# Performance work log

Measured on AMD Instinct MI355X. Metric: run time of the kernel, lower is better.

## Reference

```python
import jax, jax.numpy as jnp
import numpy as np

B, H, W, C = 16, 224, 224, 3
NP = 14                      # n_patches per side
PH = PW = H // NP            # 16
PATCH = PH * PW * C          # 768
D_MODEL = 512
EXPAND = 2
D_INNER = D_MODEL * EXPAND   # 1024
D_STATE = 16
D_CONV = 4
DT_RANK = -(-D_MODEL // 16)  # ceil(512/16) = 32
N_LAYERS = 4
N_CLASSES = 1000


def posemb_sincos_2d(h, w, dim, temperature=10000.0):
    y, x = jnp.meshgrid(jnp.arange(h, dtype=jnp.float32), jnp.arange(w, dtype=jnp.float32), indexing='ij')
    omega = jnp.arange(dim // 4, dtype=jnp.float32) / (dim // 4 - 1)
    omega = 1.0 / (temperature ** omega)
    yy = y.reshape(-1, 1) * omega[None, :]
    xx = x.reshape(-1, 1) * omega[None, :]
    return jnp.concatenate([jnp.sin(xx), jnp.cos(xx), jnp.sin(yy), jnp.cos(yy)], axis=1)  # [h*w, dim]


def setup_inputs() -> dict:
    key = jax.random.key(0)
    ks = jax.random.split(key, 12)
    s = 0.02
    inp = {
        'x': jax.random.normal(ks[0], (B, H, W, C), jnp.float32),
        'patch_w': jax.random.normal(ks[1], (PATCH, D_MODEL), jnp.float32) * s,
        'patch_b': jnp.zeros((D_MODEL,), jnp.float32),
        'norm_w': jnp.ones((N_LAYERS, D_MODEL), jnp.float32),
        'in_proj_w': jax.random.normal(ks[2], (N_LAYERS, D_MODEL, 2 * D_INNER), jnp.float32) * s,
        'conv_w': jax.random.normal(ks[3], (N_LAYERS, D_INNER, D_CONV), jnp.float32) * 0.1,
        'x_proj_w': jax.random.normal(ks[4], (N_LAYERS, D_INNER, DT_RANK + 2 * D_STATE), jnp.float32) * s,
        'dt_proj_w': jax.random.normal(ks[5], (N_LAYERS, DT_RANK, D_INNER), jnp.float32) * s,
        'dt_proj_b': jax.random.normal(ks[6], (N_LAYERS, D_INNER), jnp.float32) * 0.1,
        'A_log': jnp.broadcast_to(jnp.log(jnp.arange(1, D_STATE + 1, dtype=jnp.float32)), (N_LAYERS, D_INNER, D_STATE)) + 0.0,
        'D': jnp.ones((N_LAYERS, D_INNER), jnp.float32),
        'out_proj_w': jax.random.normal(ks[7], (N_LAYERS, D_INNER, D_MODEL), jnp.float32) * s,
        'head_w': jax.random.normal(ks[8], (D_MODEL, N_CLASSES), jnp.float32) * s,
        'head_b': jnp.zeros((N_CLASSES,), jnp.float32),
    }
    return inp


def rms_norm(x, w, eps=1e-5):
    return x * jax.lax.rsqrt(jnp.mean(x * x, axis=-1, keepdims=True) + eps) * w


def selective_scan(u, delta, A, Bm, Cm, Dv):
    # u, delta: [b,l,d]; A: [d,n]; Bm, Cm: [b,l,n]; Dv: [d]
    dA = jnp.exp(jnp.einsum('bld,dn->bldn', delta, A))          # [b,l,d,n]
    dBu = jnp.einsum('bld,bln->bldn', delta * u, Bm)            # [b,l,d,n]
    b, l, d = u.shape
    n = A.shape[1]

    def step(s, inp):
        dA_t, dBu_t, C_t = inp
        s = dA_t * s + dBu_t                                    # [b,d,n]
        y = jnp.einsum('bdn,bn->bd', s, C_t)
        return s, y

    s0 = jnp.zeros((b, d, n), u.dtype)
    _, ys = jax.lax.scan(step, s0, (dA.transpose(1, 0, 2, 3), dBu.transpose(1, 0, 2, 3), Cm.transpose(1, 0, 2)))
    y = ys.transpose(1, 0, 2)                                   # [b,l,d]
    return y + u * Dv


def mamba_block(x, in_w, conv_w, xp_w, dt_w, dt_b, A_log, Dv, out_w):
    b, l, _ = x.shape
    xr = x @ in_w                                               # [b,l,2*d_inner]
    xi, res = jnp.split(xr, 2, axis=-1)
    # causal depthwise conv over sequence
    xc = jax.lax.conv_general_dilated(
        xi.transpose(0, 2, 1),                                  # [b,d_inner,l]
        conv_w[:, None, :],                                     # [d_inner,1,k]
        window_strides=(1,), padding=[(D_CONV - 1, 0)],
        feature_group_count=D_INNER,
        dimension_numbers=('NCH', 'OIH', 'NCH'))
    xi = jax.nn.silu(xc.transpose(0, 2, 1))                     # [b,l,d_inner]
    A = -jnp.exp(A_log)
    x_dbl = xi @ xp_w                                           # [b,l,dt_rank+2n]
    delta, Bm, Cm = jnp.split(x_dbl, [DT_RANK, DT_RANK + D_STATE], axis=-1)
    delta = jax.nn.softplus(delta @ dt_w + dt_b)                # [b,l,d_inner]
    y = selective_scan(xi, delta, A, Bm, Cm, Dv)
    y = y * jax.nn.silu(res)
    return y @ out_w


def reference(x, patch_w, patch_b, norm_w, in_proj_w, conv_w, x_proj_w, dt_proj_w, dt_proj_b, A_log, D, out_proj_w, head_w, head_b):
    b = x.shape[0]
    # patchify: b (h ph) (w pw) c -> b (h w) (ph pw c)
    p = x.reshape(b, NP, PH, NP, PW, C).transpose(0, 1, 3, 2, 4, 5).reshape(b, NP * NP, PATCH)
    h = p @ patch_w + patch_b                                   # [b, 196, d_model]
    h = h + posemb_sincos_2d(NP, NP, D_MODEL)[None]
    for i in range(N_LAYERS):
        h = h + mamba_block(rms_norm(h, norm_w[i]), in_proj_w[i], conv_w[i], x_proj_w[i],
                            dt_proj_w[i], dt_proj_b[i], A_log[i], D[i], out_proj_w[i])
    h = h.mean(axis=1)                                          # [b, d_model]
    return h @ head_w + head_b                                  # [b, n_classes]
```

## Files before the change

### kernel.cpp

```cpp
#include <hip/hip_runtime.h>
#include <hip/hip_bf16.h>
#include <math.h>

#define BATCH 16
#define L_SEQ 196
#define PATCH_DIM 768
#define D_MODEL 512
#define D_INNER 1024
#define D_STATE 16
#define D_CONV 4
#define DT_RANK 32
#define N_LAYERS 4
#define N_CLASSES 1000
#define ROWS (BATCH * L_SEQ)
#define ROWSP 3200
#define NBIG 1152

typedef __hip_bfloat16 bf16;
typedef __attribute__((ext_vector_type(8))) __bf16 bf16x8;
typedef __attribute__((ext_vector_type(8))) short short8;
typedef __attribute__((ext_vector_type(4))) float f32x4;

__device__ __forceinline__ void gload_lds16(const void* g, void* l) {
    __builtin_amdgcn_global_load_lds((const __attribute__((address_space(1))) void*)g,
                                     (__attribute__((address_space(3))) void*)l, 16, 0, 0);
}
__device__ __forceinline__ float bfbits2f(int b) {
    return __int_as_float(((unsigned)b & 0xFFFFu) << 16);
}
__device__ __forceinline__ unsigned short f2bfbits(float f) {
    __hip_bfloat16 h = __float2bfloat16(f);
    return *reinterpret_cast<unsigned short*>(&h);
}

__global__ void posemb_kernel(float* __restrict__ pos) {
    int idx = blockIdx.x * 256 + threadIdx.x;
    if (idx >= L_SEQ * D_MODEL) return;
    int l = idx >> 9, col = idx & 511;
    int q = col >> 7, wi = col & 127;
    float omega = powf(10000.f, -(float)wi / 127.f);
    float yv = (float)(l / 14), xv = (float)(l % 14);
    float arg = (q < 2 ? xv : yv) * omega;
    pos[idx] = (q & 1) ? cosf(arg) : sinf(arg);
}

__global__ void patchify_kernel(const float* __restrict__ x, bf16* __restrict__ p) {
    int idx = blockIdx.x * 256 + threadIdx.x;
    if (idx >= ROWS * PATCH_DIM) return;
    int k = idx % PATCH_DIM, row = idx / PATCH_DIM;
    int b = row / L_SEQ, l = row % L_SEQ;
    int i = l / 14, j = l % 14;
    int ph = k / 48, r = k % 48, pw = r / 3, c = r % 3;
    size_t src = (((size_t)b * 224 + i * 16 + ph) * 224 + (j * 16 + pw)) * 3 + c;
    p[idx] = __float2bfloat16(x[src]);
}

__global__ __launch_bounds__(256) void transpose_bf16_kernel(
    const float* __restrict__ src, bf16* __restrict__ dst,
    int K, int N, int Npad, size_t src_lstride, size_t dst_lstride)
{
    src += (size_t)blockIdx.z * src_lstride;
    dst += (size_t)blockIdx.z * dst_lstride;
    __shared__ float tile[32][33];
    int kb = blockIdx.y * 32, nb = blockIdx.x * 32;
    int tx = threadIdx.x & 31, ty = threadIdx.x >> 5;
    #pragma unroll
    for (int i = 0; i < 4; ++i) {
        int k = kb + ty + 8 * i, n = nb + tx;
        tile[ty + 8 * i][tx] = (k < K && n < N) ? src[(size_t)k * N + n] : 0.f;
    }
    __syncthreads();
    #pragma unroll
    for (int i = 0; i < 4; ++i) {
        int n = nb + ty + 8 * i, k = kb + tx;
        if (n < Npad && k < K) dst[(size_t)n * K + k] = __float2bfloat16(tile[tx][ty + 8 * i]);
    }
}

__global__ __launch_bounds__(256) void wcomb_kernel(
    const float* __restrict__ xpw_all,
    const float* __restrict__ dtw_all,
    bf16* __restrict__ WtBig_all)
{
    int z = blockIdx.z;
    const float* xpw = xpw_all + (size_t)z * D_INNER * 64;
    const float* dtw = dtw_all + (size_t)z * DT_RANK * D_INNER;
    bf16* Wt = WtBig_all + (size_t)z * NBIG * D_INNER;
    __shared__ float sd[32][17];
    __shared__ float sx[16][33];
    int n0 = blockIdx.x * 16, k0 = blockIdx.y * 16;
    int tid = threadIdx.x;
    {
        int e = tid;        sd[e >> 4][e & 15] = dtw[(e >> 4) * D_INNER + n0 + (e & 15)];
        e = tid + 256;      sd[e >> 4][e & 15] = dtw[(e >> 4) * D_INNER + n0 + (e & 15)];
    }
    {
        int e = tid;        sx[e >> 5][e & 31] = xpw[(size_t)(k0 + (e >> 5)) * 64 + (e & 31)];
        e = tid + 256;      sx[e >> 5][e & 31] = xpw[(size_t)(k0 + (e >> 5)) * 64 + (e & 31)];
    }
    __syncthreads();
    int nn = tid >> 4, kk = tid & 15;
    float acc = 0.f;
    #pragma unroll
    for (int r = 0; r < 32; ++r) acc += sd[r][nn] * sx[kk][r];
    Wt[(size_t)(n0 + nn) * D_INNER + k0 + kk] = __float2bfloat16(acc);
}

__global__ void bcw_kernel(const float* __restrict__ xpw_all, bf16* __restrict__ WtBig_all) {
    int z = blockIdx.y;
    const float* xpw = xpw_all + (size_t)z * D_INNER * 64;
    bf16* WtBig = WtBig_all + (size_t)z * NBIG * D_INNER;
    int idx = blockIdx.x * 256 + threadIdx.x;
    if (idx >= 32 * 1024) return;
    int j = idx >> 10, k = idx & 1023;
    int src = (j & 1) ? 48 + (j >> 1) : 32 + (j >> 1);
    WtBig[(size_t)(1024 + j) * 1024 + k] = __float2bfloat16(xpw[k * 64 + src]);
}

__global__ void cwt_kernel(const float* __restrict__ cw, float* __restrict__ cwT) {
    int z = blockIdx.y;
    int idx = blockIdx.x * 256 + threadIdx.x;
    if (idx >= 4096) return;
    int d = idx >> 2, k = idx & 3;
    cwT[(size_t)z * 4096 + k * 1024 + d] = cw[(size_t)z * 4096 + d * 4 + k];
}

template<int MODE, int BM>
__global__ __launch_bounds__(256) void gemm64(
    const bf16* __restrict__ A, const bf16* __restrict__ Wt,
    int K, int gx, int Nstore, int M, int ldc,
    float* __restrict__ Cf, bf16* __restrict__ Cb,
    const float* __restrict__ bias, const float* __restrict__ pos,
    float* __restrict__ Cf2)
{
    constexpr int MI = BM / 32;
    constexpr int NL = 4 + 2 * MI;
    int nwg = gridDim.x, bid = blockIdx.x;
    int q = nwg >> 3, r = nwg & 7;
    int xcd = bid & 7, sub = bid >> 3;
    int wgid = (xcd < r ? xcd * (q + 1) : r * (q + 1) + (xcd - r) * q) + sub;
    int bx = wgid % gx, by = wgid / gx;
    int bm = by * BM, bn = bx * 128;

    __shared__ short Als[2][BM * 64];
    __shared__ short Bls[2][128 * 64];
    int tid = threadIdx.x;
    int lane = tid & 63, wid = tid >> 6;
    int wm = wid >> 1, wn = wid & 1;

    int t3 = tid >> 3, t7 = tid & 7;
    int rA0 = t3,      kA0 = t7 ^ (rA0 & 7);
    int rA1 = 32 + t3, kA1 = t7 ^ (rA1 & 7);
    const bf16* gA0 = A + (size_t)(bm + rA0) * K + kA0 * 8;
    const bf16* gA1 = A + (size_t)(bm + rA1) * K + kA1 * 8;
    const int aB0 = (wid * 64) * 8, aB1 = (256 + wid * 64) * 8;
    int rB0 = t3,      kB0 = t7 ^ (rB0 & 7);
    int rB1 = 32 + t3, kB1 = t7 ^ (rB1 & 7);
    int rB2 = 64 + t3, kB2 = t7 ^ (rB2 & 7);
    int rB3 = 96 + t3, kB3 = t7 ^ (rB3 & 7);
    const bf16* gB0 = Wt + (size_t)(bn + rB0) * K + kB0 * 8;
    const bf16* gB1 = Wt + (size_t)(bn + rB1) * K + kB1 * 8;
    const bf16* gB2 = Wt + (size_t)(bn + rB2) * K + kB2 * 8;
    const bf16* gB3 = Wt + (size_t)(bn + rB3) * K + kB3 * 8;
    const int bB0 = (wid * 64) * 8,       bB1 = (256 + wid * 64) * 8;
    const int bB2 = (512 + wid * 64) * 8, bB3 = (768 + wid * 64) * 8;

    auto stage = [&](int buf, int k0) {
        gload_lds16(gA0 + k0, &Als[buf][aB0]);
        if (BM == 64) gload_lds16(gA1 + k0, &Als[buf][aB1]);
        gload_lds16(gB0 + k0, &Bls[buf][bB0]);
        gload_lds16(gB1 + k0, &Bls[buf][bB1]);
        gload_lds16(gB2 + k0, &Bls[buf][bB2]);
        gload_lds16(gB3 + k0, &Bls[buf][bB3]);
    };

    f32x4 acc[MI][4];
    #pragma unroll
    for (int i = 0; i < MI; ++i)
        #pragma unroll
        for (int j = 0; j < 4; ++j)
            acc[i][j] = (f32x4){0.f, 0.f, 0.f, 0.f};

    stage(0, 0);
    int cur = 0;
    for (int k0 = 0; k0 < K; k0 += 64) {
        if (k0 + 64 < K) {
            stage(cur ^ 1, k0 + 64);
            __builtin_amdgcn_sched_barrier(0);
            asm volatile("s_waitcnt vmcnt(%0)" :: "n"(NL) : "memory");
        } else {
            asm volatile("s_waitcnt vmcnt(0)" ::: "memory");
        }
        __builtin_amdgcn_s_barrier();
        __builtin_amdgcn_sched_barrier(0);

        bf16x8 af[2][MI], bfr[2][4];
        #pragma unroll
        for (int kw = 0; kw < 2; ++kw) {
            int kc = kw * 4 + (lane >> 4);
            #pragma unroll
            for (int mi = 0; mi < MI; ++mi) {
                int row = wm * (BM / 2) + mi * 16 + (lane & 15);
                int kbp = kc ^ (row & 7);
                af[kw][mi] = *reinterpret_cast<const bf16x8*>(&Als[cur][row * 64 + kbp * 8]);
            }
            #pragma unroll
            for (int nj = 0; nj < 4; ++nj) {
                int row = wn * 64 + nj * 16 + (lane & 15);
                int kbp = kc ^ (row & 7);
                bfr[kw][nj] = *reinterpret_cast<const bf16x8*>(&Bls[cur][row * 64 + kbp * 8]);
            }
        }
        #pragma unroll
        for (int kw = 0; kw < 2; ++kw)
            #pragma unroll
            for (int mi = 0; mi < MI; ++mi)
                #pragma unroll
                for (int nj = 0; nj < 4; ++nj)
                    acc[mi][nj] = __builtin_amdgcn_mfma_f32_16x16x32_bf16(af[kw][mi], bfr[kw][nj], acc[mi][nj], 0, 0, 0);

        __builtin_amdgcn_sched_barrier(0);
        __builtin_amdgcn_s_barrier();
        cur ^= 1;
    }

    #pragma unroll
    for (int mi = 0; mi < MI; ++mi) {
        #pragma unroll
        for (int nj = 0; nj < 4; ++nj) {
            int r0 = bm + wm * (BM / 2) + mi * 16 + ((lane >> 4) << 2);
            int col = bn + wn * 64 + nj * 16 + (lane & 15);
            if (col >= Nstore) continue;
            #pragma unroll
            for (int j = 0; j < 4; ++j) {
                int row = r0 + j;
                if (row >= M) continue;
                float v = acc[mi][nj][j];
                if (MODE == 4) {
                    if (col < 1024) {
                        float z = v + bias[col];
                        Cf[(size_t)row * 1024 + col] = (z > 20.f) ? z : log1pf(__expf(z));
                    } else {
                        Cf2[(size_t)row * 32 + (col - 1024)] = v;
                    }
                } else {
                    size_t o = (size_t)row * ldc + col;
                    if (MODE == 0) Cb[o] = __float2bfloat16(v);
                    else if (MODE == 2) Cf[o] = v + bias[col] + pos[(size_t)(row % L_SEQ) * D_MODEL + col];
                    else if (MODE == 3) Cf[o] += v;
                }
            }
        }
    }
}

__global__ __launch_bounds__(256) void rmsnorm_kernel(
    const float* __restrict__ h, const float* __restrict__ w, bf16* __restrict__ o)
{
    int row = blockIdx.x;
    int tid = threadIdx.x;
    const float* hr = h + (size_t)row * D_MODEL;
    float v0 = hr[tid], v1 = hr[tid + 256];
    float ss = v0 * v0 + v1 * v1;
    #pragma unroll
    for (int off = 32; off; off >>= 1) ss += __shfl_down(ss, off);
    __shared__ float ls[4];
    __shared__ float scale_s;
    if ((tid & 63) == 0) ls[tid >> 6] = ss;
    __syncthreads();
    if (tid == 0) {
        float t = ls[0] + ls[1] + ls[2] + ls[3];
        scale_s = rsqrtf(t * (1.f / D_MODEL) + 1e-5f);
    }
    __syncthreads();
    float sc = scale_s;
    o[(size_t)row * D_MODEL + tid]       = __float2bfloat16(v0 * sc * w[tid]);
    o[(size_t)row * D_MODEL + tid + 256] = __float2bfloat16(v1 * sc * w[tid + 256]);
}

__global__ __launch_bounds__(256) void conv_silu_kernel(
    const bf16* __restrict__ xr, const float* __restrict__ cwT,
    bf16* __restrict__ xs, unsigned int* __restrict__ ug)
{
    int idx = blockIdx.x * 256 + threadIdx.x;
    if (idx >= ROWS * 128) return;
    int dg = idx & 127, row = idx >> 7;
    int d0 = dg << 3;
    int l = row % L_SEQ;
    float acc[8] = {0.f,0.f,0.f,0.f,0.f,0.f,0.f,0.f};
    #pragma unroll
    for (int k = 0; k < 4; ++k) {
        int ls = l - 3 + k;
        if (ls < 0) continue;
        short8 xv = *reinterpret_cast<const short8*>(xr + (size_t)(row - 3 + k) * 2048 + d0);
        const float* wk = cwT + k * 1024 + d0;
        #pragma unroll
        for (int j = 0; j < 8; ++j)
            acc[j] += bfbits2f(xv[j]) * wk[j];
    }
    short8 rv = *reinterpret_cast<const short8*>(xr + (size_t)row * 2048 + 1024 + d0);
    short8 xsv;
    unsigned ugv[8];
    #pragma unroll
    for (int j = 0; j < 8; ++j) {
        float u = acc[j] / (1.f + __expf(-acc[j]));
        unsigned short ub = f2bfbits(u);
        xsv[j] = (short)ub;
        float res = bfbits2f(rv[j]);
        float g = res / (1.f + __expf(-res));
        ugv[j] = (unsigned)ub | ((unsigned)f2bfbits(g) << 16);
    }
    *reinterpret_cast<short8*>(xs + (size_t)row * 1024 + d0) = xsv;
    uint4* up = reinterpret_cast<uint4*>(ug + (size_t)row * 1024 + d0);
    up[0] = make_uint4(ugv[0], ugv[1], ugv[2], ugv[3]);
    up[1] = make_uint4(ugv[4], ugv[5], ugv[6], ugv[7]);
}

__global__ __launch_bounds__(256) void scan_sp_kernel(
    const unsigned int* __restrict__ ug,
    const float* __restrict__ delta,
    const float* __restrict__ bc,
    const float* __restrict__ A_log,
    const float* __restrict__ Dv,
    bf16* __restrict__ y)
{
    int tid = threadIdx.x;
    int n2 = tid & 7, ch = tid >> 3;
    int b = blockIdx.x >> 5;
    int d = (((int)blockIdx.x & 31) << 5) | ch;
    size_t bbase = (size_t)b * L_SEQ;

    const float L2E = 1.4426950408889634f;
    float A0 = -__expf(A_log[d * 16 + 2 * n2]) * L2E;
    float A1 = -__expf(A_log[d * 16 + 2 * n2 + 1]) * L2E;
    float Dd = Dv[d];
    float s0 = 0.f, s1 = 0.f;

    const unsigned* pu = ug + bbase * 1024 + d;
    const float*    pd = delta + bbase * 1024 + d;
    const float*    pb = bc + bbase * 32 + 4 * n2;
    bf16*           py = y + bbase * 1024 + d;

    unsigned uv[8];
    float dlv[8];
    f32x4 bcv[8];

#define LOADSLOT(i) { \
    uv[i]  = pu[(i) * 1024]; \
    dlv[i] = pd[(i) * 1024]; \
    bcv[i] = *reinterpret_cast<const f32x4*>(pb + (i) * 32); }

#define STEP(i) { \
    float _dl = dlv[i]; \
    float _u  = __int_as_float(uv[i] << 16); \
    float _a0 = __builtin_amdgcn_exp2f(_dl * A0); \
    float _a1 = __builtin_amdgcn_exp2f(_dl * A1); \
    float _du = _dl * _u; \
    s0 = _a0 * s0 + _du * bcv[i].x; \
    s1 = _a1 * s1 + _du * bcv[i].z; \
    float _p = s0 * bcv[i].y + s1 * bcv[i].w; \
    _p += __int_as_float(__builtin_amdgcn_mov_dpp(__float_as_int(_p), 0xB1, 0xF, 0xF, true)); \
    _p += __int_as_float(__builtin_amdgcn_mov_dpp(__float_as_int(_p), 0x4E, 0xF, 0xF, true)); \
    _p += __int_as_float(__builtin_amdgcn_mov_dpp(__float_as_int(_p), 0x141, 0xF, 0xF, true)); \
    if (n2 == 0) { \
        float _g = __int_as_float(uv[i] & 0xFFFF0000u); \
        py[(i) * 1024] = __float2bfloat16((_p + _u * Dd) * _g); \
    } }

    LOADSLOT(0) LOADSLOT(1) LOADSLOT(2) LOADSLOT(3)
    LOADSLOT(4) LOADSLOT(5) LOADSLOT(6) LOADSLOT(7)
    pu += 8 * 1024; pd += 8 * 1024; pb += 8 * 32;

    for (int g = 0; g < 23; ++g) {
        STEP(0) LOADSLOT(0)
        STEP(1) LOADSLOT(1)
        STEP(2) LOADSLOT(2)
        STEP(3) LOADSLOT(3)
        STEP(4) LOADSLOT(4)
        STEP(5) LOADSLOT(5)
        STEP(6) LOADSLOT(6)
        STEP(7) LOADSLOT(7)
        pu += 8 * 1024; pd += 8 * 1024; pb += 8 * 32; py += 8 * 1024;
    }
    STEP(0) LOADSLOT(0)
    STEP(1) LOADSLOT(1)
    STEP(2) LOADSLOT(2)
    STEP(3) LOADSLOT(3)
    STEP(4) STEP(5) STEP(6) STEP(7)
    py += 8 * 1024;
    STEP(0) STEP(1) STEP(2) STEP(3)
#undef LOADSLOT
#undef STEP
}

__global__ __launch_bounds__(256) void mean_kernel(const float* __restrict__ h,
                                                   float* __restrict__ hm) {
    int c = blockIdx.x * 256 + threadIdx.x;
    int b = blockIdx.y;
    const float* hb = h + (size_t)b * L_SEQ * D_MODEL + c;
    float acc = 0.f;
    #pragma unroll 4
    for (int l = 0; l < L_SEQ; ++l) acc += hb[(size_t)l * D_MODEL];
    hm[b * D_MODEL + c] = acc * (1.f / L_SEQ);
}

__global__ __launch_bounds__(256) void head_kernel(
    const float* __restrict__ hm, const float* __restrict__ head_w,
    const float* __restrict__ head_b, float* __restrict__ out)
{
    __shared__ float hmr[D_MODEL];
    int tid = threadIdx.x;
    int b = blockIdx.y;
    hmr[tid]       = hm[b * D_MODEL + tid];
    hmr[tid + 256] = hm[b * D_MODEL + tid + 256];
    __syncthreads();
    int c = blockIdx.x * 256 + tid;
    if (c >= N_CLASSES) return;
    float acc = head_b[c];
    #pragma unroll 8
    for (int k = 0; k < D_MODEL; ++k)
        acc += hmr[k] * head_w[(size_t)k * N_CLASSES + c];
    out[(size_t)b * N_CLASSES + c] = acc;
}

extern "C" void kernel_launch(void* const* d_in, const int* in_sizes, int n_in,
                              void* d_out, int out_size, void* d_ws, size_t ws_size,
                              hipStream_t stream) {
    const float* x         = (const float*)d_in[0];
    const float* patch_w   = (const float*)d_in[1];
    const float* patch_b   = (const float*)d_in[2];
    const float* norm_w    = (const float*)d_in[3];
    const float* in_proj_w = (const float*)d_in[4];
    const float* conv_w    = (const float*)d_in[5];
    const float* x_proj_w  = (const float*)d_in[6];
    const float* dt_proj_w = (const float*)d_in[7];
    const float* dt_proj_b = (const float*)d_in[8];
    const float* A_log     = (const float*)d_in[9];
    const float* Dv        = (const float*)d_in[10];
    const float* out_proj_w= (const float*)d_in[11];
    const float* head_w    = (const float*)d_in[12];
    const float* head_b    = (const float*)d_in[13];
    float* out = (float*)d_out;

    char* base = (char*)d_ws;
    size_t off = 0;
    auto alloc = [&](size_t bytes) -> void* {
        void* p = base + off;
        off += (bytes + 255) & ~(size_t)255;
        return p;
    };
    float* pos   = (float*)alloc((size_t)L_SEQ * D_MODEL * 4);
    bf16*  pwT   = (bf16*) alloc((size_t)D_MODEL * PATCH_DIM * 2);
    bf16*  inT   = (bf16*) alloc((size_t)N_LAYERS * 2 * D_INNER * D_MODEL * 2);
    bf16*  WtBig = (bf16*) alloc((size_t)N_LAYERS * NBIG * D_INNER * 2);
    bf16*  opT   = (bf16*) alloc((size_t)N_LAYERS * D_MODEL * D_INNER * 2);
    float* cwT   = (float*)alloc((size_t)N_LAYERS * 4 * D_INNER * 4);
    float* h     = (float*)alloc((size_t)ROWS * D_MODEL * 4);
    bf16*  xn    = (bf16*) alloc((size_t)ROWSP * D_MODEL * 2);
    char*  reg0  = (char*) alloc((size_t)ROWSP * 2 * D_INNER * 2);
    bf16*  p     = (bf16*)reg0;
    bf16*  xr    = (bf16*)reg0;
    bf16*  xs    = (bf16*) alloc((size_t)ROWSP * D_INNER * 2);
    unsigned int* ug = (unsigned int*)alloc((size_t)ROWSP * D_INNER * 4);
    float* delta = (float*)alloc((size_t)ROWSP * D_INNER * 4);
    float* bcb   = (float*)alloc((size_t)ROWS * 32 * 4);
    bf16*  yb    = (bf16*) alloc((size_t)ROWSP * D_INNER * 2);
    float* hm    = (float*)alloc((size_t)BATCH * D_MODEL * 4);

    posemb_kernel<<<(L_SEQ * D_MODEL + 255) / 256, 256, 0, stream>>>(pos);
    patchify_kernel<<<(ROWS * PATCH_DIM + 255) / 256, 256, 0, stream>>>(x, p);
    transpose_bf16_kernel<<<dim3(16, 24), 256, 0, stream>>>(
        patch_w, pwT, PATCH_DIM, D_MODEL, D_MODEL, 0, 0);
    transpose_bf16_kernel<<<dim3(64, 16, N_LAYERS), 256, 0, stream>>>(
        in_proj_w, inT, D_MODEL, 2 * D_INNER, 2 * D_INNER,
        (size_t)D_MODEL * 2 * D_INNER, (size_t)2 * D_INNER * D_MODEL);
    transpose_bf16_kernel<<<dim3(16, 32, N_LAYERS), 256, 0, stream>>>(
        out_proj_w, opT, D_INNER, D_MODEL, D_MODEL,
        (size_t)D_INNER * D_MODEL, (size_t)D_MODEL * D_INNER);
    wcomb_kernel<<<dim3(64, 64, N_LAYERS), 256, 0, stream>>>(
        x_proj_w, dt_proj_w, WtBig);
    bcw_kernel<<<dim3(128, N_LAYERS), 256, 0, stream>>>(x_proj_w, WtBig);
    cwt_kernel<<<dim3(16, N_LAYERS), 256, 0, stream>>>(conv_w, cwT);

    gemm64<2, 32><<<(D_MODEL / 128) * (ROWSP / 32), 256, 0, stream>>>(
        p, pwT, PATCH_DIM, D_MODEL / 128, D_MODEL, ROWS, D_MODEL,
        h, nullptr, patch_b, pos, nullptr);

    for (int layer = 0; layer < N_LAYERS; ++layer) {
        rmsnorm_kernel<<<ROWS, 256, 0, stream>>>(h, norm_w + layer * D_MODEL, xn);

        gemm64<0, 64><<<(2 * D_INNER / 128) * (ROWSP / 64), 256, 0, stream>>>(
            xn, inT + (size_t)layer * 2 * D_INNER * D_MODEL,
            D_MODEL, 2 * D_INNER / 128, 2 * D_INNER, ROWS, 2 * D_INNER,
            nullptr, xr, nullptr, nullptr, nullptr);

        conv_silu_kernel<<<(ROWS * 128 + 255) / 256, 256, 0, stream>>>(
            xr, cwT + (size_t)layer * 4 * D_INNER, xs, ug);

        gemm64<4, 64><<<(NBIG / 128) * (ROWSP / 64), 256, 0, stream>>>(
            xs, WtBig + (size_t)layer * NBIG * D_INNER,
            D_INNER, NBIG / 128, 1056, ROWS, 0,
            delta, nullptr, dt_proj_b + (size_t)layer * D_INNER, nullptr, bcb);

        scan_sp_kernel<<<BATCH * (D_INNER / 32), 256, 0, stream>>>(
            ug, delta, bcb,
            A_log + (size_t)layer * D_INNER * D_STATE,
            Dv + (size_t)layer * D_INNER, yb);

        gemm64<3, 32><<<(D_MODEL / 128) * (ROWSP / 32), 256, 0, stream>>>(
            yb, opT + (size_t)layer * D_MODEL * D_INNER,
            D_INNER, D_MODEL / 128, D_MODEL, ROWS, D_MODEL,
            h, nullptr, nullptr, nullptr, nullptr);
    }

    mean_kernel<<<dim3(2, BATCH), 256, 0, stream>>>(h, hm);
    head_kernel<<<dim3(4, BATCH), 256, 0, stream>>>(hm, head_w, head_b, out);
}
```

Measured before the change: 552.6 us.

## Triple-buffer GEMM LDS staging and merge small prep kernels into one launch

The GEMM's K loop moves from double buffering to a three-stage LDS ring, with loads issued two steps ahead and vmcnt waits adjusted to match. This is meant to hide global-to-LDS latency better, at the cost of 1.5x the shared memory per block, which may reduce occupancy. Separately, the posemb, bcw and cwt setup kernels are folded into one launch to cut launch overhead. The NL count of outstanding loads is hardcoded to 6 or 5, which matches the number of loads each stage issues.

Measured after the change: 546.0 us. About the same (-1.2%).

```diff
diff --git a/kernel.cpp b/kernel.cpp
--- a/kernel.cpp
+++ b/kernel.cpp
@@ -33,17 +33,6 @@
     return *reinterpret_cast<unsigned short*>(&h);
 }
 
-__global__ void posemb_kernel(float* __restrict__ pos) {
-    int idx = blockIdx.x * 256 + threadIdx.x;
-    if (idx >= L_SEQ * D_MODEL) return;
-    int l = idx >> 9, col = idx & 511;
-    int q = col >> 7, wi = col & 127;
-    float omega = powf(10000.f, -(float)wi / 127.f);
-    float yv = (float)(l / 14), xv = (float)(l % 14);
-    float arg = (q < 2 ? xv : yv) * omega;
-    pos[idx] = (q & 1) ? cosf(arg) : sinf(arg);
-}
-
 __global__ void patchify_kernel(const float* __restrict__ x, bf16* __restrict__ p) {
     int idx = blockIdx.x * 256 + threadIdx.x;
     if (idx >= ROWS * PATCH_DIM) return;
@@ -53,6 +42,37 @@
     int ph = k / 48, r = k % 48, pw = r / 3, c = r % 3;
     size_t src = (((size_t)b * 224 + i * 16 + ph) * 224 + (j * 16 + pw)) * 3 + c;
     p[idx] = __float2bfloat16(x[src]);
+}
+
+__global__ void smallprep_kernel(float* __restrict__ pos,
+                                 const float* __restrict__ xpw_all,
+                                 bf16* __restrict__ WtBig_all,
+                                 const float* __restrict__ cw,
+                                 float* __restrict__ cwT) {
+    int bid = blockIdx.x, tid = threadIdx.x;
+    if (bid < 392) {
+        int idx = bid * 256 + tid;
+        if (idx >= L_SEQ * D_MODEL) return;
+        int l = idx >> 9, col = idx & 511;
+        int qd = col >> 7, wi = col & 127;
+        float omega = powf(10000.f, -(float)wi / 127.f);
+        float yv = (float)(l / 14), xv = (float)(l % 14);
+        float arg = (qd < 2 ? xv : yv) * omega;
+        pos[idx] = (qd & 1) ? cosf(arg) : sinf(arg);
+    } else if (bid < 904) {
+        int z = (bid - 392) >> 7;
+        int idx = ((bid - 392) & 127) * 256 + tid;
+        const float* xpw = xpw_all + (size_t)z * D_INNER * 64;
+        bf16* WtBig = WtBig_all + (size_t)z * NBIG * D_INNER;
+        int j = idx >> 10, k = idx & 1023;
+        int src = (j & 1) ? 48 + (j >> 1) : 32 + (j >> 1);
+        WtBig[(size_t)(1024 + j) * 1024 + k] = __float2bfloat16(xpw[k * 64 + src]);
+    } else {
+        int z = (bid - 904) >> 4;
+        int idx = ((bid - 904) & 15) * 256 + tid;
+        int d = idx >> 2, k = idx & 3;
+        cwT[(size_t)z * 4096 + k * 1024 + d] = cw[(size_t)z * 4096 + d * 4 + k];
+    }
 }
 
 __global__ __launch_bounds__(256) void transpose_bf16_kernel(
@@ -106,25 +126,6 @@
     Wt[(size_t)(n0 + nn) * D_INNER + k0 + kk] = __float2bfloat16(acc);
 }
 
-__global__ void bcw_kernel(const float* __restrict__ xpw_all, bf16* __restrict__ WtBig_all) {
-    int z = blockIdx.y;
-    const float* xpw = xpw_all + (size_t)z * D_INNER * 64;
-    bf16* WtBig = WtBig_all + (size_t)z * NBIG * D_INNER;
-    int idx = blockIdx.x * 256 + threadIdx.x;
-    if (idx >= 32 * 1024) return;
-    int j = idx >> 10, k = idx & 1023;
-    int src = (j & 1) ? 48 + (j >> 1) : 32 + (j >> 1);
-    WtBig[(size_t)(1024 + j) * 1024 + k] = __float2bfloat16(xpw[k * 64 + src]);
-}
-
-__global__ void cwt_kernel(const float* __restrict__ cw, float* __restrict__ cwT) {
-    int z = blockIdx.y;
-    int idx = blockIdx.x * 256 + threadIdx.x;
-    if (idx >= 4096) return;
-    int d = idx >> 2, k = idx & 3;
-    cwT[(size_t)z * 4096 + k * 1024 + d] = cw[(size_t)z * 4096 + d * 4 + k];
-}
-
 template<int MODE, int BM>
 __global__ __launch_bounds__(256) void gemm64(
     const bf16* __restrict__ A, const bf16* __restrict__ Wt,
@@ -134,7 +135,7 @@
     float* __restrict__ Cf2)
 {
     constexpr int MI = BM / 32;
-    constexpr int NL = 4 + 2 * MI;
+    constexpr int NL = (BM == 64) ? 6 : 5;
     int nwg = gridDim.x, bid = blockIdx.x;
     int q = nwg >> 3, r = nwg & 7;
     int xcd = bid & 7, sub = bid >> 3;
@@ -142,8 +143,8 @@
     int bx = wgid % gx, by = wgid / gx;
     int bm = by * BM, bn = bx * 128;
 
-    __shared__ short Als[2][BM * 64];
-    __shared__ short Bls[2][128 * 64];
+    __shared__ short Als[3][BM * 64];
+    __shared__ short Bls[3][128 * 64];
     int tid = threadIdx.x;
     int lane = tid & 63, wid = tid >> 6;
     int wm = wid >> 1, wn = wid & 1;
@@ -181,12 +182,17 @@
         for (int j = 0; j < 4; ++j)
             acc[i][j] = (f32x4){0.f, 0.f, 0.f, 0.f};
 
+    int nsteps = K >> 6;
     stage(0, 0);
-    int cur = 0;
-    for (int k0 = 0; k0 < K; k0 += 64) {
-        if (k0 + 64 < K) {
-            stage(cur ^ 1, k0 + 64);
+    if (nsteps > 1) stage(1, 64);
+
+    for (int s = 0; s < nsteps; ++s) {
+        int buf = s % 3;
+        if (s + 2 < nsteps) {
+            stage((s + 2) % 3, (s + 2) * 64);
             __builtin_amdgcn_sched_barrier(0);
+            asm volatile("s_waitcnt vmcnt(%0)" :: "n"(2 * NL) : "memory");
+        } else if (s + 1 < nsteps) {
             asm volatile("s_waitcnt vmcnt(%0)" :: "n"(NL) : "memory");
         } else {
             asm volatile("s_waitcnt vmcnt(0)" ::: "memory");
@@ -202,13 +208,13 @@
             for (int mi = 0; mi < MI; ++mi) {
                 int row = wm * (BM / 2) + mi * 16 + (lane & 15);
                 int kbp = kc ^ (row & 7);
-                af[kw][mi] = *reinterpret_cast<const bf16x8*>(&Als[cur][row * 64 + kbp * 8]);
+                af[kw][mi] = *reinterpret_cast<const bf16x8*>(&Als[buf][row * 64 + kbp * 8]);
             }
             #pragma unroll
             for (int nj = 0; nj < 4; ++nj) {
                 int row = wn * 64 + nj * 16 + (lane & 15);
                 int kbp = kc ^ (row & 7);
-                bfr[kw][nj] = *reinterpret_cast<const bf16x8*>(&Bls[cur][row * 64 + kbp * 8]);
+                bfr[kw][nj] = *reinterpret_cast<const bf16x8*>(&Bls[buf][row * 64 + kbp * 8]);
             }
         }
         #pragma unroll
@@ -221,7 +227,6 @@
 
         __builtin_amdgcn_sched_barrier(0);
         __builtin_amdgcn_s_barrier();
-        cur ^= 1;
     }
 
     #pragma unroll
@@ -467,8 +472,8 @@
     bf16*  yb    = (bf16*) alloc((size_t)ROWSP * D_INNER * 2);
     float* hm    = (float*)alloc((size_t)BATCH * D_MODEL * 4);
 
-    posemb_kernel<<<(L_SEQ * D_MODEL + 255) / 256, 256, 0, stream>>>(pos);
     patchify_kernel<<<(ROWS * PATCH_DIM + 255) / 256, 256, 0, stream>>>(x, p);
+    smallprep_kernel<<<968, 256, 0, stream>>>(pos, x_proj_w, WtBig, conv_w, cwT);
     transpose_bf16_kernel<<<dim3(16, 24), 256, 0, stream>>>(
         patch_w, pwT, PATCH_DIM, D_MODEL, D_MODEL, 0, 0);
     transpose_bf16_kernel<<<dim3(64, 16, N_LAYERS), 256, 0, stream>>>(
@@ -479,8 +484,6 @@
         (size_t)D_INNER * D_MODEL, (size_t)D_MODEL * D_INNER);
     wcomb_kernel<<<dim3(64, 64, N_LAYERS), 256, 0, stream>>>(
         x_proj_w, dt_proj_w, WtBig);
-    bcw_kernel<<<dim3(128, N_LAYERS), 256, 0, stream>>>(x_proj_w, WtBig);
-    cwt_kernel<<<dim3(16, N_LAYERS), 256, 0, stream>>>(conv_w, cwT);
 
     gemm64<2, 32><<<(D_MODEL / 128) * (ROWSP / 32), 256, 0, stream>>>(
         p, pwT, PATCH_DIM, D_MODEL / 128, D_MODEL, ROWS, D_MODEL,
```
